# Performance work log

Measured on AMD Instinct MI355X. Metric: run time of the kernel, lower is better.

Reference implementation:

```python
import jax, jax.numpy as jnp
import numpy as np

N_USER = 50000
N_ITEM = 50000
N_EDGE = 600000
D = 128


def _mean_agg(msg, dst, num_nodes):
    # segment-sum of messages and edge counts; nodes with no in-edges get 0 (DGL semantics)
    s = jax.ops.segment_sum(msg, dst, num_segments=num_nodes)
    cnt = jax.ops.segment_sum(jnp.ones((dst.shape[0], 1), msg.dtype), dst, num_segments=num_nodes)
    return s / jnp.maximum(cnt, 1.0)


def setup_inputs() -> dict:
    key = jax.random.key(0)
    ks = jax.random.split(key, 14)
    scale = 1.0 / np.sqrt(D)
    return {
        "feat_user": jax.random.normal(ks[0], (N_USER, D), jnp.float32),
        "feat_item": jax.random.normal(ks[1], (N_ITEM, D), jnp.float32),
        "W_uu": jax.random.normal(ks[2], (D, D), jnp.float32) * scale,
        "b_uu": jax.random.normal(ks[3], (D,), jnp.float32) * scale,
        "W_ub": jax.random.normal(ks[4], (D, D), jnp.float32) * scale,
        "b_ub": jax.random.normal(ks[5], (D,), jnp.float32) * scale,
        "W_iu": jax.random.normal(ks[6], (D, D), jnp.float32) * scale,
        "b_iu": jax.random.normal(ks[7], (D,), jnp.float32) * scale,
        "src_uu": jax.random.randint(ks[8], (N_EDGE,), 0, N_USER, jnp.int32),
        "dst_uu": jax.random.randint(ks[9], (N_EDGE,), 0, N_USER, jnp.int32),
        "src_ub": jax.random.randint(ks[10], (N_EDGE,), 0, N_USER, jnp.int32),
        "dst_ub": jax.random.randint(ks[11], (N_EDGE,), 0, N_ITEM, jnp.int32),
        "src_iu": jax.random.randint(ks[12], (N_EDGE,), 0, N_ITEM, jnp.int32),
        "dst_iu": jax.random.randint(ks[13], (N_EDGE,), 0, N_USER, jnp.int32),
    }


def reference(feat_user, feat_item, W_uu, b_uu, W_ub, b_ub, W_iu, b_iu,
              src_uu, dst_uu, src_ub, dst_ub, src_iu, dst_iu):
    # per-edge-type linear projection of src node features
    Wh_uu = feat_user @ W_uu + b_uu   # (user, follows, user)
    Wh_ub = feat_user @ W_ub + b_ub   # (user, buys, item)
    Wh_iu = feat_item @ W_iu + b_iu   # (item, bought_by, user)
    # copy_u -> mean per dst node, per edge type
    h_uu = _mean_agg(Wh_uu[src_uu], dst_uu, N_USER)
    h_ub = _mean_agg(Wh_ub[src_ub], dst_ub, N_ITEM)
    h_iu = _mean_agg(Wh_iu[src_iu], dst_iu, N_USER)
    # cross-type combine = 'sum' per dst ntype
    out_user = h_uu + h_iu
    out_item = h_ub
    return out_user, out_item
```

## Files before the change

kernel.cpp:

```cpp
#include <hip/hip_runtime.h>
#include <stdint.h>
#include <string.h>

#define N_USER 50000
#define N_ITEM 50000
#define N_EDGE 600000
#define D 128
#define NTOT 150000
#define ETOT 1800000
#define NB 293
#define BSH 9
#define SPAN 512
#define CHUNK 4096

typedef unsigned short u16;
typedef unsigned int   u32;
typedef __attribute__((ext_vector_type(8))) short short8;
typedef __attribute__((ext_vector_type(4))) float floatx4;

static __device__ __forceinline__ u16 f2b(float f) {
  u32 x; memcpy(&x, &f, 4);
  u32 r = x + 0x7fffu + ((x >> 16) & 1u);
  return (u16)(r >> 16);
}
static __device__ __forceinline__ float blo2f(u32 v) {
  u32 x = v << 16; float f; memcpy(&f, &x, 4); return f;
}
static __device__ __forceinline__ float bhi2f(u32 v) {
  u32 x = v & 0xffff0000u; float f; memcpy(&f, &x, 4); return f;
}

__global__ void __launch_bounds__(256) k_front(
    const int* __restrict__ duu, const int* __restrict__ dub, const int* __restrict__ diu,
    int* __restrict__ bhist,
    const float* __restrict__ W0, const float* __restrict__ W1, const float* __restrict__ W2,
    u16* __restrict__ WT,
    const float* __restrict__ fu, const float* __restrict__ fi,
    u16* __restrict__ fb_u, u16* __restrict__ fb_i) {
  int bid = blockIdx.x;
  if (bid < 440) {
    __shared__ int h[NB];
    for (int i = threadIdx.x; i < NB; i += 256) h[i] = 0;
    __syncthreads();
    int base = bid * CHUNK;
    for (int j = threadIdx.x; j < CHUNK; j += 256) {
      int e = base + j;
      if (e < ETOT) {
        int t = e / N_EDGE, i = e - t * N_EDGE;
        int d = (t == 0) ? duu[i] : ((t == 1) ? dub[i] : diu[i]);
        atomicAdd(&h[(t * N_USER + d) >> BSH], 1);
      }
    }
    __syncthreads();
    for (int i = threadIdx.x; i < NB; i += 256) if (h[i]) atomicAdd(&bhist[i], h[i]);
  } else if (bid < 443) {
    int wsel = bid - 440;
    for (int idx = threadIdx.x; idx < D * D; idx += 256) {
      int n = idx >> 7, k = idx & 127;
      if (wsel == 0)      WT[n * 256 + k]       = f2b(W0[k * D + n]);
      else if (wsel == 1) WT[n * 256 + 128 + k] = f2b(W2[k * D + n]);
      else                WT[32768 + n * D + k] = f2b(W1[k * D + n]);
    }
  } else {
    int base = (bid - 443) * 2048;
#pragma unroll
    for (int u = 0; u < 8; ++u) {
      int gid = base + u * 256 + threadIdx.x;
      if (gid < 3200000) {
        const float* src = fu; u16* dst = fb_u; int g = gid;
        if (g >= 1600000) { g -= 1600000; src = fi; dst = fb_i; }
        float4 v = ((const float4*)src)[g];
        union { u16 u[4]; uint2 d; } pk;
        pk.u[0] = f2b(v.x); pk.u[1] = f2b(v.y); pk.u[2] = f2b(v.z); pk.u[3] = f2b(v.w);
        ((uint2*)dst)[g] = pk.d;
      }
    }
  }
}

__global__ void __launch_bounds__(256) k_bplace(
    const int* __restrict__ suu, const int* __restrict__ duu,
    const int* __restrict__ sub, const int* __restrict__ dub,
    const int* __restrict__ siu, const int* __restrict__ diu,
    const int* __restrict__ bhist, int* __restrict__ cursor,
    int* __restrict__ boff, u32* __restrict__ ebuf) {
  __shared__ int h[NB];
  __shared__ int sboff[NB];
  __shared__ int buf[256];
  int t = threadIdx.x;
  int a = (2 * t < NB) ? bhist[2 * t] : 0;
  int b = (2 * t + 1 < NB) ? bhist[2 * t + 1] : 0;
  buf[t] = a + b; __syncthreads();
  for (int s = 1; s < 256; s <<= 1) {
    int y = (t >= s) ? buf[t - s] : 0;
    __syncthreads(); buf[t] += y; __syncthreads();
  }
  int ex = buf[t] - (a + b);
  if (2 * t < NB) sboff[2 * t] = ex;
  if (2 * t + 1 < NB) sboff[2 * t + 1] = ex + a;
  if (blockIdx.x == 0) {
    if (2 * t < NB) boff[2 * t] = ex;
    if (2 * t + 1 < NB) boff[2 * t + 1] = ex + a;
    if (t == 255) boff[NB] = buf[255];
  }
  for (int i = t; i < NB; i += 256) h[i] = 0;
  __syncthreads();
  int base = blockIdx.x * CHUNK;
  u32 pay[16], br[16];
#pragma unroll
  for (int k = 0; k < 16; ++k) {
    int e = base + k * 256 + t;
    br[k] = 0xFFFFFFFFu;
    if (e < ETOT) {
      int ty = e / N_EDGE, i = e - ty * N_EDGE;
      int d, s;
      if (ty == 0)      { d = duu[i]; s = suu[i]; }
      else if (ty == 1) { d = dub[i]; s = sub[i]; }
      else              { d = diu[i]; s = siu[i]; }
      int slot = ty * N_USER + d;
      int bu = slot >> BSH;
      int rank = atomicAdd(&h[bu], 1);
      pay[k] = (u32)s | ((u32)(slot & (SPAN - 1)) << 16);
      br[k]  = (u32)bu | ((u32)rank << 9);
    }
  }
  __syncthreads();
  for (int i = t; i < NB; i += 256)
    h[i] = sboff[i] + atomicAdd(&cursor[i], h[i]);
  __syncthreads();
#pragma unroll
  for (int k = 0; k < 16; ++k) {
    if (br[k] != 0xFFFFFFFFu) {
      int bu = br[k] & 0x1FF, rank = (int)(br[k] >> 9);
      ebuf[h[bu] + rank] = pay[k];
    }
  }
}

__global__ void __launch_bounds__(256) k_csr(const int* __restrict__ boff, const u32* __restrict__ ebuf,
                                             int* __restrict__ off, u16* __restrict__ ssrc) {
  __shared__ int sc[SPAN];
  __shared__ int so[SPAN];
  __shared__ int part[256];
  int b = blockIdx.x;
  int ebase = boff[b], ecnt = boff[b + 1] - ebase;
  int sbase = b << BSH;
  int nslots = (NTOT - sbase < SPAN) ? (NTOT - sbase) : SPAN;
  for (int i = threadIdx.x; i < SPAN; i += 256) sc[i] = 0;
  __syncthreads();
  for (int j = threadIdx.x; j < ecnt; j += 256)
    atomicAdd(&sc[ebuf[ebase + j] >> 16], 1);
  __syncthreads();
  int t = threadIdx.x;
  int s0 = sc[2 * t], s1 = sc[2 * t + 1];
  int tsum = s0 + s1;
  part[t] = tsum; __syncthreads();
  for (int s = 1; s < 256; s <<= 1) {
    int y = (t >= s) ? part[t - s] : 0;
    __syncthreads(); part[t] += y; __syncthreads();
  }
  int pbase = part[t] - tsum;
  so[2 * t]     = pbase;
  so[2 * t + 1] = pbase + s0;
  __syncthreads();
  for (int i = threadIdx.x; i < nslots; i += 256)
    off[sbase + i] = ebase + so[i];
  if (b == 0 && threadIdx.x == 0) off[NTOT] = ETOT;
  for (int i = threadIdx.x; i < SPAN; i += 256) sc[i] = so[i];
  __syncthreads();
  for (int j = threadIdx.x; j < ecnt; j += 256) {
    u32 p = ebuf[ebase + j];
    int pos = atomicAdd(&sc[p >> 16], 1);
    ssrc[ebase + pos] = (u16)(p & 0xFFFFu);
  }
}

__global__ void __launch_bounds__(256) k_mean(const u16* __restrict__ fb_u, const u16* __restrict__ fb_i,
                                              const int* __restrict__ off, const u16* __restrict__ ssrc,
                                              u16* __restrict__ ob) {
  int slot = blockIdx.x * 8 + (threadIdx.x >> 5);
  int lane = threadIdx.x & 31;
  if (slot >= NTOT) return;
  int t = slot / N_USER;
  int d = slot - t * N_USER;
  const u16* fb = (t == 2) ? fb_i : fb_u;
  int s = off[slot], e = off[slot + 1];
  int n = e - s;
  int my_src = (lane < n) ? (int)ssrc[s + lane] : 0;
  float a0 = 0.f, a1 = 0.f, a2 = 0.f, a3 = 0.f;
  int m = (n < 32) ? n : 32;
  int i = 0;
  for (; i + 4 <= m; i += 4) {
    int s0 = __shfl(my_src, i, 32);
    int s1 = __shfl(my_src, i + 1, 32);
    int s2 = __shfl(my_src, i + 2, 32);
    int s3 = __shfl(my_src, i + 3, 32);
    uint2 v0 = ((const uint2*)(fb + (size_t)s0 * D))[lane];
    uint2 v1 = ((const uint2*)(fb + (size_t)s1 * D))[lane];
    uint2 v2 = ((const uint2*)(fb + (size_t)s2 * D))[lane];
    uint2 v3 = ((const uint2*)(fb + (size_t)s3 * D))[lane];
    a0 += blo2f(v0.x) + blo2f(v1.x) + blo2f(v2.x) + blo2f(v3.x);
    a1 += bhi2f(v0.x) + bhi2f(v1.x) + bhi2f(v2.x) + bhi2f(v3.x);
    a2 += blo2f(v0.y) + blo2f(v1.y) + blo2f(v2.y) + blo2f(v3.y);
    a3 += bhi2f(v0.y) + bhi2f(v1.y) + bhi2f(v2.y) + bhi2f(v3.y);
  }
  for (; i < m; ++i) {
    int sr = __shfl(my_src, i, 32);
    uint2 v = ((const uint2*)(fb + (size_t)sr * D))[lane];
    a0 += blo2f(v.x); a1 += bhi2f(v.x);
    a2 += blo2f(v.y); a3 += bhi2f(v.y);
  }
  for (int j = s + 32; j < e; ++j) {
    int sr = ssrc[j];
    uint2 v = ((const uint2*)(fb + (size_t)sr * D))[lane];
    a0 += blo2f(v.x); a1 += bhi2f(v.x);
    a2 += blo2f(v.y); a3 += bhi2f(v.y);
  }
  float inv = (n > 0) ? 1.0f / (float)n : 0.f;
  u32 p0 = (u32)f2b(a0 * inv) | ((u32)f2b(a1 * inv) << 16);
  u32 p1 = (u32)f2b(a2 * inv) | ((u32)f2b(a3 * inv) << 16);
  u32* mrow;
  if (t == 0)      mrow = (u32*)(ob + (size_t)d * 256);
  else if (t == 2) mrow = (u32*)(ob + (size_t)d * 256 + 128);
  else             mrow = (u32*)(ob + 12800000 + (size_t)d * 256);
  ((uint2*)mrow)[lane] = make_uint2(p0, p1);
}

__global__ void __launch_bounds__(256, 2) k_out(float* out, const u16* __restrict__ WT,
                                                const float* __restrict__ buu, const float* __restrict__ bub,
                                                const float* __restrict__ biu, const int* __restrict__ off) {
  int users = (blockIdx.y == 0);
  int tid = threadIdx.x;
  int w = tid >> 6, lane = tid & 63, quad = lane >> 4, l16 = lane & 15;
  int KT = users ? 8 : 4;
  const u16* Wsrc = users ? WT : (WT + 32768);
  int wstride = users ? 256 : 128;

  __shared__ u16 sB[32768];
  int nfrag = KT * 8 * 64;
  for (int fid = tid; fid < nfrag; fid += 256) {
    int fl = fid & 63, fnt = (fid >> 6) & 7, fkk = fid >> 9;
    int fq = fl >> 4, fl16 = fl & 15;
    const u16* src = Wsrc + (fnt * 16 + fl16) * wstride + fkk * 32 + fq * 8;
    *(uint4*)(sB + (size_t)fid * 8) = *(const uint4*)src;
  }

  int row0 = blockIdx.x * 128 + w * 32;
  const u16* ob = (const u16*)out;
  const u16* Abase = users ? ob : (ob + 12800000);
  size_t outoff = users ? 0 : (size_t)N_USER;

  int r0a = row0 + l16, r1a = row0 + 16 + l16;
  int rA0 = r0a < N_USER ? r0a : N_USER - 1;
  int rA1 = r1a < N_USER ? r1a : N_USER - 1;
  const u16* A0 = Abase + (size_t)rA0 * 256 + quad * 8;
  const u16* A1 = Abase + (size_t)rA1 * 256 + quad * 8;

  short8 af0[8], af1[8];
#pragma unroll
  for (int kk = 0; kk < 8; ++kk) {
    if (kk < KT) {
      af0[kk] = *(const short8*)(A0 + kk * 32);
      af1[kk] = *(const short8*)(A1 + kk * 32);
    }
  }
  int nA[2][4], nB[2][4];
#pragma unroll
  for (int rt = 0; rt < 2; ++rt)
#pragma unroll
    for (int i = 0; i < 4; ++i) {
      int grow = row0 + rt * 16 + quad * 4 + i;
      bool ok = grow < N_USER;
      if (users) {
        nA[rt][i] = ok ? (off[grow + 1] - off[grow]) : 0;
        nB[rt][i] = ok ? (off[2 * N_USER + grow + 1] - off[2 * N_USER + grow]) : 0;
      } else {
        nA[rt][i] = ok ? (off[N_USER + grow + 1] - off[N_USER + grow]) : 0;
        nB[rt][i] = 0;
      }
    }
  __syncthreads();

  floatx4 acc[2][8];
#pragma unroll
  for (int rt = 0; rt < 2; ++rt)
#pragma unroll
    for (int nt = 0; nt < 8; ++nt) acc[rt][nt] = (floatx4){0.f, 0.f, 0.f, 0.f};

#pragma unroll
  for (int kk = 0; kk < 8; ++kk) {
    if (kk < KT) {
      const short8* bp = (const short8*)(sB + ((size_t)kk * 512 + lane) * 8);
#pragma unroll
      for (int nt = 0; nt < 8; ++nt) {
        short8 bf = bp[nt * 64];
        acc[0][nt] = __builtin_amdgcn_mfma_f32_16x16x32_bf16(af0[kk], bf, acc[0][nt], 0, 0, 0);
        acc[1][nt] = __builtin_amdgcn_mfma_f32_16x16x32_bf16(af1[kk], bf, acc[1][nt], 0, 0, 0);
      }
    }
  }

#pragma unroll
  for (int rt = 0; rt < 2; ++rt) {
    int tbase = row0 + rt * 16;
#pragma unroll
    for (int nt = 0; nt < 8; ++nt) {
      int col = nt * 16 + l16;
      float bA = users ? buu[col] : bub[col];
      float bB = users ? biu[col] : 0.f;
#pragma unroll
      for (int i = 0; i < 4; ++i) {
        int grow = tbase + quad * 4 + i;
        if (grow < N_USER) {
          float r = acc[rt][nt][i] + (nA[rt][i] > 0 ? bA : 0.f) + (nB[rt][i] > 0 ? bB : 0.f);
          out[(outoff + (size_t)grow) * D + col] = r;
        }
      }
    }
  }
}

extern "C" void kernel_launch(void* const* d_in, const int* in_sizes, int n_in,
                              void* d_out, int out_size, void* d_ws, size_t ws_size,
                              hipStream_t stream) {
  const float* fu  = (const float*)d_in[0];
  const float* fi  = (const float*)d_in[1];
  const float* Wuu = (const float*)d_in[2];
  const float* buu = (const float*)d_in[3];
  const float* Wub = (const float*)d_in[4];
  const float* bub = (const float*)d_in[5];
  const float* Wiu = (const float*)d_in[6];
  const float* biu = (const float*)d_in[7];
  const int* suu = (const int*)d_in[8];
  const int* duu = (const int*)d_in[9];
  const int* sub = (const int*)d_in[10];
  const int* dub = (const int*)d_in[11];
  const int* siu = (const int*)d_in[12];
  const int* diu = (const int*)d_in[13];
  float* out = (float*)d_out;
  u16* ob = (u16*)d_out;

  int* wsi    = (int*)d_ws;
  int* off    = wsi;
  int* bhist  = wsi + 150016;
  int* cursor = wsi + 150336;
  int* boff   = wsi + 150656;
  u32* ebuf   = (u32*)(wsi + 150976);
  u16* ssrc   = (u16*)(wsi + 1950976);
  u16* WT     = (u16*)(wsi + 2850976);
  u16* fb_u   = (u16*)(wsi + 2875552);
  u16* fb_i   = (u16*)(wsi + 6075552);

  hipMemsetAsync(bhist, 0, 640 * sizeof(int), stream);
  k_front<<<443 + 1563, 256, 0, stream>>>(duu, dub, diu, bhist, Wuu, Wub, Wiu, WT,
                                          fu, fi, fb_u, fb_i);
  k_bplace<<<440, 256, 0, stream>>>(suu, duu, sub, dub, siu, diu, bhist, cursor, boff, ebuf);
  k_csr<<<NB, 256, 0, stream>>>(boff, ebuf, off, ssrc);
  k_mean<<<18750, 256, 0, stream>>>(fb_u, fb_i, off, ssrc, ob);
  k_out<<<dim3(391, 2), 256, 0, stream>>>(out, WT, buu, bub, biu, off);
}
```

Before: 279.9 us.

## Spread feature bf16 conversion across bplace and csr kernels; unroll gather by 8

```diff
diff --git a/kernel.cpp b/kernel.cpp
--- a/kernel.cpp
+++ b/kernel.cpp
@@ -30,13 +30,28 @@
   u32 x = v & 0xffff0000u; float f; memcpy(&f, &x, 4); return f;
 }
 
+static __device__ __forceinline__ void conv_chunk(int cbase,
+    const float* __restrict__ fu, const float* __restrict__ fi,
+    u16* __restrict__ fb_u, u16* __restrict__ fb_i) {
+#pragma unroll
+  for (int u = 0; u < 8; ++u) {
+    int gid = cbase + u * 256 + (int)threadIdx.x;
+    if (gid < 3200000) {
+      const float* src = fu; u16* dst = fb_u; int g = gid;
+      if (g >= 1600000) { g -= 1600000; src = fi; dst = fb_i; }
+      float4 v = ((const float4*)src)[g];
+      union { u16 q[4]; uint2 d; } pk;
+      pk.q[0] = f2b(v.x); pk.q[1] = f2b(v.y); pk.q[2] = f2b(v.z); pk.q[3] = f2b(v.w);
+      ((uint2*)dst)[g] = pk.d;
+    }
+  }
+}
+
 __global__ void __launch_bounds__(256) k_front(
     const int* __restrict__ duu, const int* __restrict__ dub, const int* __restrict__ diu,
     int* __restrict__ bhist,
     const float* __restrict__ W0, const float* __restrict__ W1, const float* __restrict__ W2,
-    u16* __restrict__ WT,
-    const float* __restrict__ fu, const float* __restrict__ fi,
-    u16* __restrict__ fb_u, u16* __restrict__ fb_i) {
+    u16* __restrict__ WT) {
   int bid = blockIdx.x;
   if (bid < 440) {
     __shared__ int h[NB];
@@ -53,7 +68,7 @@
     }
     __syncthreads();
     for (int i = threadIdx.x; i < NB; i += 256) if (h[i]) atomicAdd(&bhist[i], h[i]);
-  } else if (bid < 443) {
+  } else {
     int wsel = bid - 440;
     for (int idx = threadIdx.x; idx < D * D; idx += 256) {
       int n = idx >> 7, k = idx & 127;
@@ -61,20 +76,6 @@
       else if (wsel == 1) WT[n * 256 + 128 + k] = f2b(W2[k * D + n]);
       else                WT[32768 + n * D + k] = f2b(W1[k * D + n]);
     }
-  } else {
-    int base = (bid - 443) * 2048;
-#pragma unroll
-    for (int u = 0; u < 8; ++u) {
-      int gid = base + u * 256 + threadIdx.x;
-      if (gid < 3200000) {
-        const float* src = fu; u16* dst = fb_u; int g = gid;
-        if (g >= 1600000) { g -= 1600000; src = fi; dst = fb_i; }
-        float4 v = ((const float4*)src)[g];
-        union { u16 u[4]; uint2 d; } pk;
-        pk.u[0] = f2b(v.x); pk.u[1] = f2b(v.y); pk.u[2] = f2b(v.z); pk.u[3] = f2b(v.w);
-        ((uint2*)dst)[g] = pk.d;
-      }
-    }
   }
 }
 
@@ -83,7 +84,13 @@
     const int* __restrict__ sub, const int* __restrict__ dub,
     const int* __restrict__ siu, const int* __restrict__ diu,
     const int* __restrict__ bhist, int* __restrict__ cursor,
-    int* __restrict__ boff, u32* __restrict__ ebuf) {
+    int* __restrict__ boff, u32* __restrict__ ebuf,
+    const float* __restrict__ fu, const float* __restrict__ fi,
+    u16* __restrict__ fb_u, u16* __restrict__ fb_i) {
+  if (blockIdx.x >= 440) {
+    conv_chunk((blockIdx.x - 440) * 2048, fu, fi, fb_u, fb_i);
+    return;
+  }
   __shared__ int h[NB];
   __shared__ int sboff[NB];
   __shared__ int buf[256];
@@ -138,7 +145,13 @@
 }
 
 __global__ void __launch_bounds__(256) k_csr(const int* __restrict__ boff, const u32* __restrict__ ebuf,
-                                             int* __restrict__ off, u16* __restrict__ ssrc) {
+                                             int* __restrict__ off, u16* __restrict__ ssrc,
+                                             const float* __restrict__ fu, const float* __restrict__ fi,
+                                             u16* __restrict__ fb_u, u16* __restrict__ fb_i) {
+  if (blockIdx.x >= NB) {
+    conv_chunk((blockIdx.x - NB) * 2048 + 1601536, fu, fi, fb_u, fb_i);
+    return;
+  }
   __shared__ int sc[SPAN];
   __shared__ int so[SPAN];
   __shared__ int part[256];
@@ -190,6 +203,19 @@
   float a0 = 0.f, a1 = 0.f, a2 = 0.f, a3 = 0.f;
   int m = (n < 32) ? n : 32;
   int i = 0;
+  for (; i + 8 <= m; i += 8) {
+    int sA[8];
+#pragma unroll
+    for (int k = 0; k < 8; ++k) sA[k] = __shfl(my_src, i + k, 32);
+    uint2 v[8];
+#pragma unroll
+    for (int k = 0; k < 8; ++k) v[k] = ((const uint2*)(fb + (size_t)sA[k] * D))[lane];
+#pragma unroll
+    for (int k = 0; k < 8; ++k) {
+      a0 += blo2f(v[k].x); a1 += bhi2f(v[k].x);
+      a2 += blo2f(v[k].y); a3 += bhi2f(v[k].y);
+    }
+  }
   for (; i + 4 <= m; i += 4) {
     int s0 = __shfl(my_src, i, 32);
     int s1 = __shfl(my_src, i + 1, 32);
@@ -352,10 +378,10 @@
   u16* fb_i   = (u16*)(wsi + 6075552);
 
   hipMemsetAsync(bhist, 0, 640 * sizeof(int), stream);
-  k_front<<<443 + 1563, 256, 0, stream>>>(duu, dub, diu, bhist, Wuu, Wub, Wiu, WT,
-                                          fu, fi, fb_u, fb_i);
-  k_bplace<<<440, 256, 0, stream>>>(suu, duu, sub, dub, siu, diu, bhist, cursor, boff, ebuf);
-  k_csr<<<NB, 256, 0, stream>>>(boff, ebuf, off, ssrc);
+  k_front<<<443, 256, 0, stream>>>(duu, dub, diu, bhist, Wuu, Wub, Wiu, WT);
+  k_bplace<<<440 + 782, 256, 0, stream>>>(suu, duu, sub, dub, siu, diu, bhist, cursor,
+                                          boff, ebuf, fu, fi, fb_u, fb_i);
+  k_csr<<<NB + 781, 256, 0, stream>>>(boff, ebuf, off, ssrc, fu, fi, fb_u, fb_i);
   k_mean<<<18750, 256, 0, stream>>>(fb_u, fb_i, off, ssrc, ob);
   k_out<<<dim3(391, 2), 256, 0, stream>>>(out, WT, buu, bub, biu, off);
 }
```

Measured after the change: 272.7 us. -2.6%, faster.
